# Performance work log

Measured on AMD Instinct MI355X. Metric: run time of the kernel, lower is better.

The kernel has to match this reference:

```python
import jax, jax.numpy as jnp
import numpy as np

DIM = 1024
HEADS = 16
DIM_HEAD = DIM // HEADS  # 64


def setup_inputs() -> dict:
    key = jax.random.key(0)
    k1, k2, k3 = jax.random.split(key, 3)
    x = jax.random.normal(k1, (4, 2048, DIM), dtype=jnp.float32)
    # Linear weights stored as [in, out] so y = x @ W (torch Linear uses x @ W.T; init is random either way)
    w_qkv = jax.random.normal(k2, (DIM, 3 * DIM), dtype=jnp.float32) * (DIM ** -0.5)
    w_out = jax.random.normal(k3, (DIM, DIM), dtype=jnp.float32) * (DIM ** -0.5)
    return {"x": x, "w_qkv": w_qkv, "w_out": w_out}


def reference(x, w_qkv, w_out):
    b, t, d = x.shape
    h, dh = HEADS, DIM_HEAD
    qkv = x @ w_qkv  # [b, t, 3*h*dh]
    q, k, v = jnp.split(qkv, 3, axis=-1)
    split_heads = lambda a: a.reshape(b, t, h, dh).transpose(0, 2, 1, 3)  # [b,h,t,dh]
    q, k, v = map(split_heads, (q, k, v))
    # NOTE: original scales by full model dim d, not per-head dim
    scale = d ** (-0.5)
    dots = jnp.einsum('bhie,bhje->bhij', q, k) * scale  # [b,h,t,t]
    attn = jax.nn.softmax(dots, axis=-1)
    out = jnp.einsum('bhij,bhje->bhie', attn, v)  # [b,h,t,dh]
    out = out.transpose(0, 2, 1, 3).reshape(b, t, h * dh)
    return out @ w_out
```

## Files before the change

kernel.cpp:

```cpp
#include <hip/hip_runtime.h>


typedef __bf16 bf16x8 __attribute__((ext_vector_type(8)));
typedef __bf16 bf16x4 __attribute__((ext_vector_type(4)));
typedef __bf16 bf16x2 __attribute__((ext_vector_type(2)));
typedef float f32x4 __attribute__((ext_vector_type(4)));
typedef float f32x2 __attribute__((ext_vector_type(2)));
typedef float f32x16 __attribute__((ext_vector_type(16)));
typedef unsigned short ushort8 __attribute__((ext_vector_type(8)));

#define MFMA16(a, b, c) __builtin_amdgcn_mfma_f32_16x16x32_bf16((a), (b), (c), 0, 0, 0)
#define MFMA32(a, b, c) __builtin_amdgcn_mfma_f32_32x32x16_bf16((a), (b), (c), 0, 0, 0)

__device__ __forceinline__ unsigned short f2bf(float f) {
  unsigned int u = __float_as_uint(f);
  u = (u + 0x7FFFu + ((u >> 16) & 1u)) >> 16;
  return (unsigned short)u;
}

__device__ __forceinline__ float fast_exp2(float x) {
#if __has_builtin(__builtin_amdgcn_exp2f)
  return __builtin_amdgcn_exp2f(x);
#else
  float r;
  asm("v_exp_f32 %0, %1" : "=v"(r) : "v"(x));
  return r;
#endif
}

__device__ __forceinline__ void gload_lds16(const unsigned short* g, unsigned short* l) {
  __builtin_amdgcn_global_load_lds(
      (const __attribute__((address_space(1))) unsigned int*)g,
      (__attribute__((address_space(3))) unsigned int*)l, 16, 0, 0);
}

__global__ __launch_bounds__(256) void prep_kernel(
    const float* __restrict__ x, unsigned short* __restrict__ xb,
    const float* __restrict__ wqkv, unsigned short* __restrict__ WqkvT,
    const float* __restrict__ wout, unsigned short* __restrict__ WoutT) {
  const int bid = blockIdx.x;
  const int tid = threadIdx.x;
  if (bid < 4096) {
    int i = (bid * 256 + tid) * 8;
    float4 a = *(const float4*)&x[i];
    float4 b = *(const float4*)&x[i + 4];
    ushort8 o = {f2bf(a.x), f2bf(a.y), f2bf(a.z), f2bf(a.w),
                 f2bf(b.x), f2bf(b.y), f2bf(b.z), f2bf(b.w)};
    *(ushort8*)&xb[i] = o;
    return;
  }
  __shared__ float t[32][33];
  const float* in;
  unsigned short* out;
  int C, scale_limit, c0, r0;
  if (bid < 4096 + 3072) {
    int tj = bid - 4096;
    in = wqkv; out = WqkvT; C = 3072; scale_limit = 1024;
    c0 = (tj % 96) * 32; r0 = (tj / 96) * 32;
  } else {
    int tj = bid - 7168;
    in = wout; out = WoutT; C = 1024; scale_limit = 0;
    c0 = (tj & 31) * 32; r0 = (tj >> 5) * 32;
  }
  const float kQScale = 0.045084220027780106f;
#pragma unroll
  for (int i = 0; i < 4; ++i) {
    int e = tid + i * 256;
    int r = e >> 5, c = e & 31;
    t[r][c] = in[(size_t)(r0 + r) * C + c0 + c];
  }
  __syncthreads();
#pragma unroll
  for (int i = 0; i < 4; ++i) {
    int e = tid + i * 256;
    int r = e >> 5, c = e & 31;
    float v = t[c][r];
    if (c0 + r < scale_limit) v *= kQScale;
    out[(size_t)(c0 + r) * 1024 + r0 + c] = f2bf(v);
  }
}

template <int MODE>
__global__ __launch_bounds__(256) void gemm_bt(
    const unsigned short* __restrict__ A, const unsigned short* __restrict__ Bt,
    void* __restrict__ Cv, unsigned short* __restrict__ VT,
    int M, int N, int K) {
  __shared__ unsigned short As[128 * 32];
  __shared__ unsigned short Bs[128 * 32];
  const int tid = threadIdx.x;
  const int wave = tid >> 6, lane = tid & 63;
  const int g = lane >> 4, ln = lane & 15;
  const int wm = wave >> 1, wn = wave & 1;
  const long bm = (long)blockIdx.y * 128;
  const long bn = (long)blockIdx.x * 128;

  f32x4 acc[4][4];
#pragma unroll
  for (int i = 0; i < 4; ++i)
#pragma unroll
    for (int j = 0; j < 4; ++j) acc[i][j] = (f32x4){0.f, 0.f, 0.f, 0.f};

  const int srow = wave * 32 + (lane >> 2);
  const int scol = (lane & 3) * 8;
  const unsigned short* gA0 = A + (bm + srow) * (long)K + scol;
  const unsigned short* gA1 = gA0 + 16 * (long)K;
  const unsigned short* gB0 = Bt + (bn + srow) * (long)K + scol;
  const unsigned short* gB1 = gB0 + 16 * (long)K;
  unsigned short* lA0 = &As[wave * 1024];
  unsigned short* lA1 = &As[wave * 1024 + 512];
  unsigned short* lB0 = &Bs[wave * 1024];
  unsigned short* lB1 = &Bs[wave * 1024 + 512];

  for (int k0 = 0; k0 < K; k0 += 32) {
    __syncthreads();
    gload_lds16(gA0 + k0, lA0);
    gload_lds16(gA1 + k0, lA1);
    gload_lds16(gB0 + k0, lB0);
    gload_lds16(gB1 + k0, lB1);
    __syncthreads();

    bf16x8 af[4], bfr[4];
#pragma unroll
    for (int i = 0; i < 4; ++i) {
      af[i]  = *(const bf16x8*)&As[(wm * 64 + i * 16 + ln) * 32 + g * 8];
      bfr[i] = *(const bf16x8*)&Bs[(wn * 64 + i * 16 + ln) * 32 + g * 8];
    }
    __builtin_amdgcn_s_setprio(1);
#pragma unroll
    for (int i = 0; i < 4; ++i)
#pragma unroll
      for (int j = 0; j < 4; ++j)
        acc[i][j] = MFMA16(af[i], bfr[j], acc[i][j]);
    __builtin_amdgcn_s_setprio(0);
  }

  const long crow = bm + wm * 64, ccol = bn + wn * 64;
  if (MODE == 2 && bn >= 2048) {
#pragma unroll
    for (int i = 0; i < 4; ++i)
#pragma unroll
      for (int j = 0; j < 4; ++j) {
        int nv = (int)(ccol + j * 16 + ln) - 2048;
        int h = nv >> 6, dh = nv & 63;
        long tg = crow + i * 16 + g * 4;
        int b = (int)(tg >> 11), tl = (int)(tg & 2047);
        size_t idx = (size_t)(b * 16 + h) * 131072 + (size_t)dh * 2048 + tl;
        bf16x4 o = {(__bf16)acc[i][j][0], (__bf16)acc[i][j][1],
                    (__bf16)acc[i][j][2], (__bf16)acc[i][j][3]};
        *(bf16x4*)&VT[idx] = o;
      }
  } else {
#pragma unroll
    for (int i = 0; i < 4; ++i)
#pragma unroll
      for (int j = 0; j < 4; ++j)
#pragma unroll
        for (int r = 0; r < 4; ++r) {
          long idx = (crow + i * 16 + g * 4 + r) * (long)N + ccol + j * 16 + ln;
          if (MODE == 1)
            ((float*)Cv)[idx] = acc[i][j][r];
          else
            ((unsigned short*)Cv)[idx] = f2bf(acc[i][j][r]);
        }
  }
}

__global__ __launch_bounds__(256, 4) void attn_kernel(
    const unsigned short* __restrict__ qkv, const unsigned short* __restrict__ VT,
    unsigned short* __restrict__ attn_out) {
  __shared__ unsigned short Ks[64][64];
  __shared__ unsigned short Vs[64][64];

  const int tid = threadIdx.x;
  const int wave = tid >> 6, lane = tid & 63;
  const int l31 = lane & 31, hb = lane >> 5;

  const int wg = (blockIdx.x & 7) * 128 + (blockIdx.x >> 3);
  const int bh = wg >> 4, qc = wg & 15;
  const int b = bh >> 4, head = bh & 15;
  const int q0 = qc * 128 + wave * 32;

  bf16x8 qf[4];
  {
    size_t base = (size_t)(b * 2048 + q0 + l31) * 3072 + head * 64 + 8 * hb;
    qf[0] = *(const bf16x8*)&qkv[base];
    qf[1] = *(const bf16x8*)&qkv[base + 16];
    qf[2] = *(const bf16x8*)&qkv[base + 32];
    qf[3] = *(const bf16x8*)&qkv[base + 48];
  }

  f32x16 oacc[2];
#pragma unroll
  for (int i = 0; i < 16; ++i) { oacc[0][i] = 0.f; oacc[1][i] = 0.f; }
  f32x2 ls = {0.f, 0.f};

  const int srow = tid >> 3;
  const int sc = tid & 7;
  const int swc = (sc ^ (srow & 7)) * 8;
  const unsigned short* gK =
      qkv + (size_t)b * 2048 * 3072 + 1024 + head * 64 + (size_t)srow * 3072 + sc * 8;
  const unsigned short* gV = VT + (size_t)bh * 131072 + (size_t)srow * 2048 + sc * 8;

  const int myx = l31 & 7;

  for (int j0 = 0; j0 < 2048; j0 += 64) {
    __syncthreads();
    *(ushort8*)&Ks[srow][swc]      = *(const ushort8*)(gK + (size_t)j0 * 3072);
    *(ushort8*)&Ks[srow + 32][swc] = *(const ushort8*)(gK + (size_t)(j0 + 32) * 3072);
    *(ushort8*)&Vs[srow][swc]      = *(const ushort8*)(gV + j0);
    *(ushort8*)&Vs[srow + 32][swc] = *(const ushort8*)(gV + 32 * 2048 + j0);
    __syncthreads();

#pragma unroll
    for (int kt = 0; kt < 2; ++kt) {
      f32x16 sa;
#pragma unroll
      for (int i = 0; i < 16; ++i) sa[i] = 0.f;
      __builtin_amdgcn_s_setprio(1);
#pragma unroll
      for (int t = 0; t < 4; ++t) {
        bf16x8 kf = *(const bf16x8*)&Ks[kt * 32 + l31][((2 * t + hb) ^ myx) * 8];
        sa = MFMA32(kf, qf[t], sa);
      }
      __builtin_amdgcn_s_setprio(0);

      unsigned int pkw[8], opk[8];
#pragma unroll
      for (int j = 0; j < 8; ++j) {
        float p0 = fast_exp2(sa[2 * j]);
        float p1 = fast_exp2(sa[2 * j + 1]);
        ls += (f32x2){p0, p1};
        bf16x2 pv = {(__bf16)p0, (__bf16)p1};
        pkw[j] = __builtin_bit_cast(unsigned int, pv);
      }
#pragma unroll
      for (int j = 0; j < 8; ++j) opk[j] = (unsigned int)__shfl_xor((int)pkw[j], 32);

      const bool H = (hb != 0);
      union { unsigned int u[4]; bf16x8 v; } pf0, pf1;
      pf0.u[0] = H ? opk[2] : pkw[0];
      pf0.u[1] = H ? opk[3] : pkw[1];
      pf0.u[2] = H ? pkw[2] : opk[0];
      pf0.u[3] = H ? pkw[3] : opk[1];
      pf1.u[0] = H ? opk[6] : pkw[4];
      pf1.u[1] = H ? opk[7] : pkw[5];
      pf1.u[2] = H ? pkw[6] : opk[4];
      pf1.u[3] = H ? pkw[7] : opk[5];

      __builtin_amdgcn_s_setprio(1);
#pragma unroll
      for (int mt = 0; mt < 2; ++mt) {
        bf16x8 vf0 = *(const bf16x8*)&Vs[mt * 32 + l31][((4 * kt + hb) ^ myx) * 8];
        bf16x8 vf1 = *(const bf16x8*)&Vs[mt * 32 + l31][((4 * kt + 2 + hb) ^ myx) * 8];
        oacc[mt] = MFMA32(vf0, pf0.v, oacc[mt]);
        oacc[mt] = MFMA32(vf1, pf1.v, oacc[mt]);
      }
      __builtin_amdgcn_s_setprio(0);
    }
  }

  float l = ls.x + ls.y;
  l += __shfl_xor(l, 32);
  float inv = 1.0f / l;
  size_t row = (size_t)(b * 2048 + q0 + l31) * 1024 + head * 64;
#pragma unroll
  for (int mt = 0; mt < 2; ++mt)
#pragma unroll
    for (int rq = 0; rq < 4; ++rq) {
      bf16x4 o = {(__bf16)(oacc[mt][4 * rq + 0] * inv),
                  (__bf16)(oacc[mt][4 * rq + 1] * inv),
                  (__bf16)(oacc[mt][4 * rq + 2] * inv),
                  (__bf16)(oacc[mt][4 * rq + 3] * inv)};
      *(bf16x4*)&attn_out[row + mt * 32 + 8 * rq + 4 * hb] = o;
    }
}

extern "C" void kernel_launch(void* const* d_in, const int* in_sizes, int n_in,
                              void* d_out, int out_size, void* d_ws, size_t ws_size,
                              hipStream_t stream) {
  (void)in_sizes; (void)n_in; (void)out_size; (void)ws_size;
  const float* x_f     = (const float*)d_in[0];
  const float* w_qkv_f = (const float*)d_in[1];
  const float* w_out_f = (const float*)d_in[2];
  float* out = (float*)d_out;

  char* ws = (char*)d_ws;
  unsigned short* qkv   = (unsigned short*)(ws);
  unsigned short* attn  = (unsigned short*)(ws + 50331648);
  unsigned short* VT    = (unsigned short*)(ws + 67108864);
  unsigned short* WqkvT = (unsigned short*)(ws + 83886080);
  unsigned short* WoutT = (unsigned short*)(ws + 90177536);
  unsigned short* xb    = (unsigned short*)(ws + 92274688);

  prep_kernel<<<8192, 256, 0, stream>>>(x_f, xb, w_qkv_f, WqkvT, w_out_f, WoutT);
  gemm_bt<2><<<dim3(24, 64), 256, 0, stream>>>(xb, WqkvT, qkv, VT, 8192, 3072, 1024);
  attn_kernel<<<1024, 256, 0, stream>>>(qkv, VT, attn);
  gemm_bt<1><<<dim3(8, 64), 256, 0, stream>>>(attn, WoutT, out, nullptr, 8192, 1024, 1024);
}
```

Baseline: 196.9 us.

## Double-buffer K/V tiles with async global-to-LDS loads and permlane32 swap

The attention loop now stages K and V tiles into two LDS buffers using direct global-to-LDS loads. The next tile's load is issued before computing on the current one, so memory latency overlaps the MFMA and exp work and the loop needs one barrier per iteration instead of two. The swizzle moves from the LDS write address to the global read address. The P-fragment half exchange also replaces eight cross-lane shuffles and selects with four permlane32_swap operations where that builtin exists. The cost is doubled LDS per block, which could reduce occupancy at 4 blocks per CU.

```diff
diff --git a/kernel.cpp b/kernel.cpp
--- a/kernel.cpp
+++ b/kernel.cpp
@@ -32,6 +32,21 @@
   __builtin_amdgcn_global_load_lds(
       (const __attribute__((address_space(1))) unsigned int*)g,
       (__attribute__((address_space(3))) unsigned int*)l, 16, 0, 0);
+}
+
+__device__ __forceinline__ void half_swap(unsigned int a, unsigned int b,
+                                          unsigned int& x, unsigned int& y,
+                                          bool H) {
+#if __has_builtin(__builtin_amdgcn_permlane32_swap)
+  auto r = __builtin_amdgcn_permlane32_swap(a, b, false, false);
+  x = (unsigned int)r[0];
+  y = (unsigned int)r[1];
+#else
+  unsigned int oa = (unsigned int)__shfl_xor((int)a, 32);
+  unsigned int ob = (unsigned int)__shfl_xor((int)b, 32);
+  x = H ? ob : a;
+  y = H ? b : oa;
+#endif
 }
 
 __global__ __launch_bounds__(256) void prep_kernel(
@@ -168,8 +183,8 @@
 __global__ __launch_bounds__(256, 4) void attn_kernel(
     const unsigned short* __restrict__ qkv, const unsigned short* __restrict__ VT,
     unsigned short* __restrict__ attn_out) {
-  __shared__ unsigned short Ks[64][64];
-  __shared__ unsigned short Vs[64][64];
+  __shared__ unsigned short Ks[2][64][64];
+  __shared__ unsigned short Vs[2][64][64];
 
   const int tid = threadIdx.x;
   const int wave = tid >> 6, lane = tid & 63;
@@ -196,20 +211,29 @@
 
   const int srow = tid >> 3;
   const int sc = tid & 7;
-  const int swc = (sc ^ (srow & 7)) * 8;
+  const int swz = (sc ^ (srow & 7)) * 8;
   const unsigned short* gK =
-      qkv + (size_t)b * 2048 * 3072 + 1024 + head * 64 + (size_t)srow * 3072 + sc * 8;
-  const unsigned short* gV = VT + (size_t)bh * 131072 + (size_t)srow * 2048 + sc * 8;
+      qkv + (size_t)b * 2048 * 3072 + 1024 + head * 64 + (size_t)srow * 3072 + swz;
+  const unsigned short* gV = VT + (size_t)bh * 131072 + (size_t)srow * 2048 + swz;
+  const int wrow = wave * 8;
+
+  auto STAGE = [&](int buf, int j) {
+    gload_lds16(gK + (size_t)j * 3072,        &Ks[buf][wrow][0]);
+    gload_lds16(gK + (size_t)(j + 32) * 3072, &Ks[buf][wrow + 32][0]);
+    gload_lds16(gV + j,                       &Vs[buf][wrow][0]);
+    gload_lds16(gV + 32 * 2048 + j,           &Vs[buf][wrow + 32][0]);
+  };
 
   const int myx = l31 & 7;
-
+  const bool H = (hb != 0);
+
+  STAGE(0, 0);
+  asm volatile("s_waitcnt vmcnt(0)" ::: "memory");
+  __syncthreads();
+
+  int cur = 0;
   for (int j0 = 0; j0 < 2048; j0 += 64) {
-    __syncthreads();
-    *(ushort8*)&Ks[srow][swc]      = *(const ushort8*)(gK + (size_t)j0 * 3072);
-    *(ushort8*)&Ks[srow + 32][swc] = *(const ushort8*)(gK + (size_t)(j0 + 32) * 3072);
-    *(ushort8*)&Vs[srow][swc]      = *(const ushort8*)(gV + j0);
-    *(ushort8*)&Vs[srow + 32][swc] = *(const ushort8*)(gV + 32 * 2048 + j0);
-    __syncthreads();
+    if (j0 + 64 < 2048) STAGE(cur ^ 1, j0 + 64);
 
 #pragma unroll
     for (int kt = 0; kt < 2; ++kt) {
@@ -219,12 +243,12 @@
       __builtin_amdgcn_s_setprio(1);
 #pragma unroll
       for (int t = 0; t < 4; ++t) {
-        bf16x8 kf = *(const bf16x8*)&Ks[kt * 32 + l31][((2 * t + hb) ^ myx) * 8];
+        bf16x8 kf = *(const bf16x8*)&Ks[cur][kt * 32 + l31][((2 * t + hb) ^ myx) * 8];
         sa = MFMA32(kf, qf[t], sa);
       }
       __builtin_amdgcn_s_setprio(0);
 
-      unsigned int pkw[8], opk[8];
+      unsigned int pkw[8];
 #pragma unroll
       for (int j = 0; j < 8; ++j) {
         float p0 = fast_exp2(sa[2 * j]);
@@ -233,30 +257,27 @@
         bf16x2 pv = {(__bf16)p0, (__bf16)p1};
         pkw[j] = __builtin_bit_cast(unsigned int, pv);
       }
-#pragma unroll
-      for (int j = 0; j < 8; ++j) opk[j] = (unsigned int)__shfl_xor((int)pkw[j], 32);
-
-      const bool H = (hb != 0);
+
       union { unsigned int u[4]; bf16x8 v; } pf0, pf1;
-      pf0.u[0] = H ? opk[2] : pkw[0];
-      pf0.u[1] = H ? opk[3] : pkw[1];
-      pf0.u[2] = H ? pkw[2] : opk[0];
-      pf0.u[3] = H ? pkw[3] : opk[1];
-      pf1.u[0] = H ? opk[6] : pkw[4];
-      pf1.u[1] = H ? opk[7] : pkw[5];
-      pf1.u[2] = H ? pkw[6] : opk[4];
-      pf1.u[3] = H ? pkw[7] : opk[5];
+      half_swap(pkw[0], pkw[2], pf0.u[0], pf0.u[2], H);
+      half_swap(pkw[1], pkw[3], pf0.u[1], pf0.u[3], H);
+      half_swap(pkw[4], pkw[6], pf1.u[0], pf1.u[2], H);
+      half_swap(pkw[5], pkw[7], pf1.u[1], pf1.u[3], H);
 
       __builtin_amdgcn_s_setprio(1);
 #pragma unroll
       for (int mt = 0; mt < 2; ++mt) {
-        bf16x8 vf0 = *(const bf16x8*)&Vs[mt * 32 + l31][((4 * kt + hb) ^ myx) * 8];
-        bf16x8 vf1 = *(const bf16x8*)&Vs[mt * 32 + l31][((4 * kt + 2 + hb) ^ myx) * 8];
+        bf16x8 vf0 = *(const bf16x8*)&Vs[cur][mt * 32 + l31][((4 * kt + hb) ^ myx) * 8];
+        bf16x8 vf1 = *(const bf16x8*)&Vs[cur][mt * 32 + l31][((4 * kt + 2 + hb) ^ myx) * 8];
         oacc[mt] = MFMA32(vf0, pf0.v, oacc[mt]);
         oacc[mt] = MFMA32(vf1, pf1.v, oacc[mt]);
       }
       __builtin_amdgcn_s_setprio(0);
     }
+
+    asm volatile("s_waitcnt vmcnt(0)" ::: "memory");
+    __syncthreads();
+    cur ^= 1;
   }
 
   float l = ls.x + ls.y;
```

Result: faster. 187.0 us (-5.1%).
